# Kernel optimization log

Hardware: AMD Instinct MI355X
Metric: run time of the kernel (lower is better)

## Reference

```python
import jax, jax.numpy as jnp
import numpy as np

N = 8192
PERCENT_ON = 0.1
K = int(round(N * PERCENT_ON))  # 819
BOOST_STRENGTH = 1.0


def setup_inputs() -> dict:
    key = jax.random.key(0)
    k1, k2 = jax.random.split(key)
    x = jax.random.normal(k1, (4096, N), dtype=jnp.float32)
    duty_cycles = jax.random.uniform(k2, (N,), dtype=jnp.float32) * 0.2
    return {"x": x, "duty_cycles": duty_cycles}


def reference(x, duty_cycles):
    # boost factors: exp((target_density - duty_cycle) * boost_strength)
    boost_strength = jnp.maximum(jnp.float32(BOOST_STRENGTH), 0.0)
    target_density = jnp.float32(K / N)
    boost_factors = jnp.exp((target_density - duty_cycles) * boost_strength)
    boosted = x * boost_factors  # [B, N]
    # top-k on boosted values, but transmit ORIGINAL x values at winning units
    _, idx = jax.lax.top_k(boosted, K)  # idx: [B, K]
    updates = jnp.take_along_axis(x, idx, axis=1)  # [B, K]
    rows = jnp.arange(x.shape[0])[:, None]  # [B, 1]
    out = jnp.zeros_like(x).at[rows, idx].set(updates)
    return out
```

## Files before the change

kernel.cpp:

```cpp
#include <hip/hip_runtime.h>
#include <math.h>

#define NCOL 8192
#define NROW 4096
#define KSEL 819
#define TPB  256
#define VPT  8
#define LCAP 256
#define KPIV 0xBF866666u
#define NBKT 2048

typedef float f32x4 __attribute__((ext_vector_type(4)));

__device__ __align__(16) float g_boost[NCOL];

__global__ void boost_kernel(const float* __restrict__ duty) {
    int i = blockIdx.x * blockDim.x + threadIdx.x;
    if (i < NCOL) {
        float diff = (0.0999755859375f - duty[i]);
        g_boost[i] = (float)exp((double)diff);
    }
}

__device__ __forceinline__ unsigned f2k(float f) {
    unsigned u = __float_as_uint(f);
    return u ^ (0x80000000u | (unsigned)((int)u >> 31));
}

__device__ __forceinline__ int kbucket(unsigned k) {
    int b = (int)(k >> 13) - (int)(KPIV >> 13);
    return (b > NBKT - 1) ? (NBKT - 1) : b;
}

__global__ __launch_bounds__(TPB) void kwinners_kernel(const float* __restrict__ x,
                                                       float* __restrict__ out) {
    __shared__ __align__(16) unsigned char smem[16384];
    __shared__ int lds_wtot[4];
    __shared__ int lds_C, lds_cnt, lds_sel, lds_R1, lds_fE, lds_fR;
    __shared__ unsigned lds_th;

    int* hist = (int*)smem;
    unsigned* lkey = (unsigned*)(smem + 8192);

    const int t = threadIdx.x, row = blockIdx.x, lane = t & 63, w = t >> 6;
    const f32x4* x4 = (const f32x4*)(x + (size_t)row * NCOL);
    const f32x4* b4 = (const f32x4*)g_boost;

    unsigned kr[VPT][4];

    {
        int4* h4 = (int4*)hist;
        const int4 z = make_int4(0, 0, 0, 0);
        h4[2 * t] = z; h4[2 * t + 1] = z;
        if (t == 0) { lds_C = 0; lds_cnt = 0; lds_th = 0xFFFFFFFFu; }
    }

#pragma unroll
    for (int j = 0; j < VPT; ++j) {
        f32x4 xx = x4[t + TPB * j];
        f32x4 bb = b4[t + TPB * j];
        kr[j][0] = f2k(xx.x * bb.x);
        kr[j][1] = f2k(xx.y * bb.y);
        kr[j][2] = f2k(xx.z * bb.z);
        kr[j][3] = f2k(xx.w * bb.w);
    }
    __syncthreads();

    int cnt = 0;
#pragma unroll
    for (int j = 0; j < VPT; ++j)
#pragma unroll
        for (int c = 0; c < 4; ++c) {
            unsigned k = kr[j][c];
            if (k > KPIV) { ++cnt; atomicAdd(&hist[kbucket(k)], 1); }
        }
#pragma unroll
    for (int off = 32; off; off >>= 1) cnt += __shfl_down(cnt, off);
    if (lane == 0) atomicAdd(&lds_C, cnt);
    __syncthreads();
    const int C = lds_C;

    unsigned th = 0; int Rf = 0, E = 0; bool ok = false;

    if (C >= KSEL) {
        int arr[8];
        {
            int4 a0 = ((const int4*)hist)[2 * t];
            int4 a1 = ((const int4*)hist)[2 * t + 1];
            arr[0] = a0.x; arr[1] = a0.y; arr[2] = a0.z; arr[3] = a0.w;
            arr[4] = a1.x; arr[5] = a1.y; arr[6] = a1.z; arr[7] = a1.w;
        }
        int ts = arr[0] + arr[1] + arr[2] + arr[3] + arr[4] + arr[5] + arr[6] + arr[7];
        int s = ts;
#pragma unroll
        for (int off = 1; off < 64; off <<= 1) {
            int o = __shfl_down(s, off);
            if (lane + off < 64) s += o;
        }
        if (lane == 0) lds_wtot[w] = s;
        __syncthreads();
        int S_later = 0;
#pragma unroll
        for (int w2 = 0; w2 < 4; ++w2) if (w2 > w) S_later += lds_wtot[w2];
        const int S_ab = (s - ts) + S_later;
        if (S_ab < KSEL && S_ab + ts >= KSEL) {
            int cum = S_ab, selb = 0, r1 = 0;
#pragma unroll
            for (int b = 7; b >= 0; --b) {
                int nx = cum + arr[b];
                if (cum < KSEL && nx >= KSEL) { selb = 8 * t + b; r1 = KSEL - cum; }
                cum = nx;
            }
            lds_sel = selb; lds_R1 = r1;
        }
        __syncthreads();
        const int sel = lds_sel, R1 = lds_R1;

#pragma unroll
        for (int j = 0; j < VPT; ++j)
#pragma unroll
            for (int c = 0; c < 4; ++c) {
                unsigned k = kr[j][c];
                if (kbucket(k) == sel) {
                    int sl = atomicAdd(&lds_cnt, 1);
                    if (sl < LCAP) lkey[sl] = k;
                }
            }
        __syncthreads();
        const int n = lds_cnt;
        if (n <= LCAP) {
            if (t < n) {
                unsigned myk = lkey[t];
                int g = 0, e = 0;
                for (int i = 0; i < n; ++i) {
                    unsigned k2 = lkey[i];
                    g += (k2 > myk) ? 1 : 0;
                    e += (k2 == myk) ? 1 : 0;
                }
                if (g < R1 && g + e >= R1) lds_th = myk;
            }
            __syncthreads();
            th = lds_th;
            int ge = 0;
#pragma unroll
            for (int j = 0; j < VPT; ++j)
#pragma unroll
                for (int c = 0; c < 4; ++c) {
                    unsigned k = kr[j][c];
                    ge += (k > th ? 1 : 0) + (k == th ? (1 << 16) : 0);
                }
#pragma unroll
            for (int off = 32; off; off >>= 1) ge += __shfl_down(ge, off);
            if (lane == 0) lds_wtot[w] = ge;
            __syncthreads();
            const int GE = lds_wtot[0] + lds_wtot[1] + lds_wtot[2] + lds_wtot[3];
            const int G = GE & 0xFFFF, Eg = GE >> 16;
            if (G < KSEL && G + Eg >= KSEL) { ok = true; Rf = KSEL - G; E = Eg; }
        }
    }

    if (!ok) {
        unsigned prefix = 0; int R = KSEL;
        for (int p = 0; p < 4; ++p) {
            const int sh = 24 - 8 * p;
            hist[t] = 0;
            __syncthreads();
#pragma unroll
            for (int j = 0; j < VPT; ++j)
#pragma unroll
                for (int c = 0; c < 4; ++c) {
                    unsigned k = kr[j][c];
                    if (p == 0 || (k >> (sh + 8)) == (prefix >> (sh + 8)))
                        atomicAdd(&hist[(k >> sh) & 255u], 1);
                }
            __syncthreads();
            int h = hist[t], s2 = h;
#pragma unroll
            for (int off = 1; off < 64; off <<= 1) {
                int o = __shfl_down(s2, off);
                if (lane + off < 64) s2 += o;
            }
            if (lane == 0) lds_wtot[w] = s2;
            __syncthreads();
            int S_later = 0;
#pragma unroll
            for (int w2 = 0; w2 < 4; ++w2) if (w2 > w) S_later += lds_wtot[w2];
            const int S_ab = (s2 - h) + S_later;
            if (S_ab < R && S_ab + h >= R) { lds_sel = t; lds_fR = R - S_ab; lds_fE = h; }
            __syncthreads();
            prefix |= ((unsigned)lds_sel) << sh;
            R = lds_fR;
        }
        th = prefix; Rf = R; E = lds_fE;
    }

    unsigned dropm = 0;
    if (E > Rf) {
        unsigned short* tl = (unsigned short*)smem;
        __syncthreads();
        if (t == 0) lds_cnt = 0;
        __syncthreads();
#pragma unroll
        for (int j = 0; j < VPT; ++j)
#pragma unroll
            for (int c = 0; c < 4; ++c)
                if (kr[j][c] == th) {
                    int sl = atomicAdd(&lds_cnt, 1);
                    tl[sl] = (unsigned short)(4 * (t + TPB * j) + c);
                }
        __syncthreads();
        const int ntie = lds_cnt;
#pragma unroll
        for (int j = 0; j < VPT; ++j)
#pragma unroll
            for (int c = 0; c < 4; ++c)
                if (kr[j][c] == th) {
                    const int col = 4 * (t + TPB * j) + c;
                    int rank = 0;
                    for (int i = 0; i < ntie; ++i) rank += (tl[i] < col) ? 1 : 0;
                    if (rank >= Rf) dropm |= (1u << (4 * j + c));
                }
    }

    f32x4* o4 = (f32x4*)(out + (size_t)row * NCOL);
#pragma unroll
    for (int j = 0; j < VPT; ++j) {
        f32x4 xx = x4[t + TPB * j];
        f32x4 r;
        r.x = (kr[j][0] >= th && !((dropm >> (4 * j + 0)) & 1u)) ? xx.x : 0.0f;
        r.y = (kr[j][1] >= th && !((dropm >> (4 * j + 1)) & 1u)) ? xx.y : 0.0f;
        r.z = (kr[j][2] >= th && !((dropm >> (4 * j + 2)) & 1u)) ? xx.z : 0.0f;
        r.w = (kr[j][3] >= th && !((dropm >> (4 * j + 3)) & 1u)) ? xx.w : 0.0f;
        __builtin_nontemporal_store(r, &o4[t + TPB * j]);
    }
}

extern "C" void kernel_launch(void* const* d_in, const int* in_sizes, int n_in,
                              void* d_out, int out_size, void* d_ws, size_t ws_size,
                              hipStream_t stream) {
    const float* x = (const float*)d_in[0];
    const float* duty = (const float*)d_in[1];
    float* out = (float*)d_out;
    (void)in_sizes; (void)n_in; (void)out_size; (void)d_ws; (void)ws_size;

    boost_kernel<<<(NCOL + TPB - 1) / TPB, TPB, 0, stream>>>(duty);
    kwinners_kernel<<<NROW, TPB, 0, stream>>>(x, out);
}
```

Measured before the change: 63.76 us.

## Process two rows per block and stagger block start with a sleep

Each block now handles two rows in sequence, and the grid is halved. At start, each block spins on wall_clock64 with s_sleep for a hash-derived delay, so blocks enter their memory-heavy and compute phases at different times instead of all at once. The aim is to cut launch overhead and to spread load/compute phases across CUs for better overlap. The cost is fewer blocks for latency hiding, deliberate idle time at the start of most blocks, and an extra barrier between rows.

Measured after the change: 70.80 us. +11.0%, slower.

```diff
diff --git a/kernel.cpp b/kernel.cpp
--- a/kernel.cpp
+++ b/kernel.cpp
@@ -6,6 +6,7 @@
 #define KSEL 819
 #define TPB  256
 #define VPT  8
+#define RPB  2
 #define LCAP 256
 #define KPIV 0xBF866666u
 #define NBKT 2048
@@ -42,196 +43,211 @@
     int* hist = (int*)smem;
     unsigned* lkey = (unsigned*)(smem + 8192);
 
-    const int t = threadIdx.x, row = blockIdx.x, lane = t & 63, w = t >> 6;
-    const f32x4* x4 = (const f32x4*)(x + (size_t)row * NCOL);
+    const int t = threadIdx.x, lane = t & 63, w = t >> 6;
     const f32x4* b4 = (const f32x4*)g_boost;
 
-    unsigned kr[VPT][4];
-
     {
-        int4* h4 = (int4*)hist;
-        const int4 z = make_int4(0, 0, 0, 0);
-        h4[2 * t] = z; h4[2 * t + 1] = z;
-        if (t == 0) { lds_C = 0; lds_cnt = 0; lds_th = 0xFFFFFFFFu; }
+        const unsigned ph = ((unsigned)blockIdx.x * 2654435761u) >> 29;
+        if (ph) {
+            long long t0 = wall_clock64();
+            const long long tgt = (long long)ph * 40;
+            while (wall_clock64() - t0 < tgt) __builtin_amdgcn_s_sleep(8);
+        }
     }
 
-#pragma unroll
-    for (int j = 0; j < VPT; ++j) {
-        f32x4 xx = x4[t + TPB * j];
-        f32x4 bb = b4[t + TPB * j];
-        kr[j][0] = f2k(xx.x * bb.x);
-        kr[j][1] = f2k(xx.y * bb.y);
-        kr[j][2] = f2k(xx.z * bb.z);
-        kr[j][3] = f2k(xx.w * bb.w);
-    }
-    __syncthreads();
-
-    int cnt = 0;
-#pragma unroll
-    for (int j = 0; j < VPT; ++j)
-#pragma unroll
-        for (int c = 0; c < 4; ++c) {
-            unsigned k = kr[j][c];
-            if (k > KPIV) { ++cnt; atomicAdd(&hist[kbucket(k)], 1); }
-        }
-#pragma unroll
-    for (int off = 32; off; off >>= 1) cnt += __shfl_down(cnt, off);
-    if (lane == 0) atomicAdd(&lds_C, cnt);
-    __syncthreads();
-    const int C = lds_C;
-
-    unsigned th = 0; int Rf = 0, E = 0; bool ok = false;
-
-    if (C >= KSEL) {
-        int arr[8];
+    for (int r = 0; r < RPB; ++r) {
+        const int row = blockIdx.x * RPB + r;
+        const f32x4* x4 = (const f32x4*)(x + (size_t)row * NCOL);
+
+        unsigned kr[VPT][4];
+
         {
-            int4 a0 = ((const int4*)hist)[2 * t];
-            int4 a1 = ((const int4*)hist)[2 * t + 1];
-            arr[0] = a0.x; arr[1] = a0.y; arr[2] = a0.z; arr[3] = a0.w;
-            arr[4] = a1.x; arr[5] = a1.y; arr[6] = a1.z; arr[7] = a1.w;
-        }
-        int ts = arr[0] + arr[1] + arr[2] + arr[3] + arr[4] + arr[5] + arr[6] + arr[7];
-        int s = ts;
-#pragma unroll
-        for (int off = 1; off < 64; off <<= 1) {
-            int o = __shfl_down(s, off);
-            if (lane + off < 64) s += o;
-        }
-        if (lane == 0) lds_wtot[w] = s;
+            int4* h4 = (int4*)hist;
+            const int4 z = make_int4(0, 0, 0, 0);
+            h4[2 * t] = z; h4[2 * t + 1] = z;
+            if (t == 0) { lds_C = 0; lds_cnt = 0; lds_th = 0xFFFFFFFFu; }
+        }
+
+#pragma unroll
+        for (int j = 0; j < VPT; ++j) {
+            f32x4 xx = x4[t + TPB * j];
+            f32x4 bb = b4[t + TPB * j];
+            kr[j][0] = f2k(xx.x * bb.x);
+            kr[j][1] = f2k(xx.y * bb.y);
+            kr[j][2] = f2k(xx.z * bb.z);
+            kr[j][3] = f2k(xx.w * bb.w);
+        }
         __syncthreads();
-        int S_later = 0;
-#pragma unroll
-        for (int w2 = 0; w2 < 4; ++w2) if (w2 > w) S_later += lds_wtot[w2];
-        const int S_ab = (s - ts) + S_later;
-        if (S_ab < KSEL && S_ab + ts >= KSEL) {
-            int cum = S_ab, selb = 0, r1 = 0;
-#pragma unroll
-            for (int b = 7; b >= 0; --b) {
-                int nx = cum + arr[b];
-                if (cum < KSEL && nx >= KSEL) { selb = 8 * t + b; r1 = KSEL - cum; }
-                cum = nx;
-            }
-            lds_sel = selb; lds_R1 = r1;
-        }
-        __syncthreads();
-        const int sel = lds_sel, R1 = lds_R1;
-
+
+        int cnt = 0;
 #pragma unroll
         for (int j = 0; j < VPT; ++j)
 #pragma unroll
             for (int c = 0; c < 4; ++c) {
                 unsigned k = kr[j][c];
-                if (kbucket(k) == sel) {
-                    int sl = atomicAdd(&lds_cnt, 1);
-                    if (sl < LCAP) lkey[sl] = k;
-                }
-            }
+                if (k > KPIV) { ++cnt; atomicAdd(&hist[kbucket(k)], 1); }
+            }
+#pragma unroll
+        for (int off = 32; off; off >>= 1) cnt += __shfl_down(cnt, off);
+        if (lane == 0) atomicAdd(&lds_C, cnt);
         __syncthreads();
-        const int n = lds_cnt;
-        if (n <= LCAP) {
-            if (t < n) {
-                unsigned myk = lkey[t];
-                int g = 0, e = 0;
-                for (int i = 0; i < n; ++i) {
-                    unsigned k2 = lkey[i];
-                    g += (k2 > myk) ? 1 : 0;
-                    e += (k2 == myk) ? 1 : 0;
-                }
-                if (g < R1 && g + e >= R1) lds_th = myk;
-            }
-            __syncthreads();
-            th = lds_th;
-            int ge = 0;
+        const int C = lds_C;
+
+        unsigned th = 0; int Rf = 0, E = 0; bool ok = false;
+
+        if (C >= KSEL) {
+            int arr[8];
+            {
+                int4 a0 = ((const int4*)hist)[2 * t];
+                int4 a1 = ((const int4*)hist)[2 * t + 1];
+                arr[0] = a0.x; arr[1] = a0.y; arr[2] = a0.z; arr[3] = a0.w;
+                arr[4] = a1.x; arr[5] = a1.y; arr[6] = a1.z; arr[7] = a1.w;
+            }
+            int ts = arr[0] + arr[1] + arr[2] + arr[3] + arr[4] + arr[5] + arr[6] + arr[7];
+            int s = ts;
+#pragma unroll
+            for (int off = 1; off < 64; off <<= 1) {
+                int o = __shfl_down(s, off);
+                if (lane + off < 64) s += o;
+            }
+            if (lane == 0) lds_wtot[w] = s;
+            __syncthreads();
+            int S_later = 0;
+#pragma unroll
+            for (int w2 = 0; w2 < 4; ++w2) if (w2 > w) S_later += lds_wtot[w2];
+            const int S_ab = (s - ts) + S_later;
+            if (S_ab < KSEL && S_ab + ts >= KSEL) {
+                int cum = S_ab, selb = 0, r1 = 0;
+#pragma unroll
+                for (int b = 7; b >= 0; --b) {
+                    int nx = cum + arr[b];
+                    if (cum < KSEL && nx >= KSEL) { selb = 8 * t + b; r1 = KSEL - cum; }
+                    cum = nx;
+                }
+                lds_sel = selb; lds_R1 = r1;
+            }
+            __syncthreads();
+            const int sel = lds_sel, R1 = lds_R1;
+
 #pragma unroll
             for (int j = 0; j < VPT; ++j)
 #pragma unroll
                 for (int c = 0; c < 4; ++c) {
                     unsigned k = kr[j][c];
-                    ge += (k > th ? 1 : 0) + (k == th ? (1 << 16) : 0);
-                }
-#pragma unroll
-            for (int off = 32; off; off >>= 1) ge += __shfl_down(ge, off);
-            if (lane == 0) lds_wtot[w] = ge;
-            __syncthreads();
-            const int GE = lds_wtot[0] + lds_wtot[1] + lds_wtot[2] + lds_wtot[3];
-            const int G = GE & 0xFFFF, Eg = GE >> 16;
-            if (G < KSEL && G + Eg >= KSEL) { ok = true; Rf = KSEL - G; E = Eg; }
-        }
-    }
-
-    if (!ok) {
-        unsigned prefix = 0; int R = KSEL;
-        for (int p = 0; p < 4; ++p) {
-            const int sh = 24 - 8 * p;
-            hist[t] = 0;
+                    if (kbucket(k) == sel) {
+                        int sl = atomicAdd(&lds_cnt, 1);
+                        if (sl < LCAP) lkey[sl] = k;
+                    }
+                }
+            __syncthreads();
+            const int n = lds_cnt;
+            if (n <= LCAP) {
+                if (t < n) {
+                    unsigned myk = lkey[t];
+                    int g = 0, e = 0;
+                    for (int i = 0; i < n; ++i) {
+                        unsigned k2 = lkey[i];
+                        g += (k2 > myk) ? 1 : 0;
+                        e += (k2 == myk) ? 1 : 0;
+                    }
+                    if (g < R1 && g + e >= R1) lds_th = myk;
+                }
+                __syncthreads();
+                th = lds_th;
+                int ge = 0;
+#pragma unroll
+                for (int j = 0; j < VPT; ++j)
+#pragma unroll
+                    for (int c = 0; c < 4; ++c) {
+                        unsigned k = kr[j][c];
+                        ge += (k > th ? 1 : 0) + (k == th ? (1 << 16) : 0);
+                    }
+#pragma unroll
+                for (int off = 32; off; off >>= 1) ge += __shfl_down(ge, off);
+                if (lane == 0) lds_wtot[w] = ge;
+                __syncthreads();
+                const int GE = lds_wtot[0] + lds_wtot[1] + lds_wtot[2] + lds_wtot[3];
+                const int G = GE & 0xFFFF, Eg = GE >> 16;
+                if (G < KSEL && G + Eg >= KSEL) { ok = true; Rf = KSEL - G; E = Eg; }
+            }
+        }
+
+        if (!ok) {
+            unsigned prefix = 0; int R = KSEL;
+            for (int p = 0; p < 4; ++p) {
+                const int sh = 24 - 8 * p;
+                hist[t] = 0;
+                __syncthreads();
+#pragma unroll
+                for (int j = 0; j < VPT; ++j)
+#pragma unroll
+                    for (int c = 0; c < 4; ++c) {
+                        unsigned k = kr[j][c];
+                        if (p == 0 || (k >> (sh + 8)) == (prefix >> (sh + 8)))
+                            atomicAdd(&hist[(k >> sh) & 255u], 1);
+                    }
+                __syncthreads();
+                int h = hist[t], s2 = h;
+#pragma unroll
+                for (int off = 1; off < 64; off <<= 1) {
+                    int o = __shfl_down(s2, off);
+                    if (lane + off < 64) s2 += o;
+                }
+                if (lane == 0) lds_wtot[w] = s2;
+                __syncthreads();
+                int S_later = 0;
+#pragma unroll
+                for (int w2 = 0; w2 < 4; ++w2) if (w2 > w) S_later += lds_wtot[w2];
+                const int S_ab = (s2 - h) + S_later;
+                if (S_ab < R && S_ab + h >= R) { lds_sel = t; lds_fR = R - S_ab; lds_fE = h; }
+                __syncthreads();
+                prefix |= ((unsigned)lds_sel) << sh;
+                R = lds_fR;
+            }
+            th = prefix; Rf = R; E = lds_fE;
+        }
+
+        unsigned dropm = 0;
+        if (E > Rf) {
+            unsigned short* tl = (unsigned short*)smem;
+            __syncthreads();
+            if (t == 0) lds_cnt = 0;
             __syncthreads();
 #pragma unroll
             for (int j = 0; j < VPT; ++j)
 #pragma unroll
-                for (int c = 0; c < 4; ++c) {
-                    unsigned k = kr[j][c];
-                    if (p == 0 || (k >> (sh + 8)) == (prefix >> (sh + 8)))
-                        atomicAdd(&hist[(k >> sh) & 255u], 1);
-                }
-            __syncthreads();
-            int h = hist[t], s2 = h;
-#pragma unroll
-            for (int off = 1; off < 64; off <<= 1) {
-                int o = __shfl_down(s2, off);
-                if (lane + off < 64) s2 += o;
-            }
-            if (lane == 0) lds_wtot[w] = s2;
-            __syncthreads();
-            int S_later = 0;
-#pragma unroll
-            for (int w2 = 0; w2 < 4; ++w2) if (w2 > w) S_later += lds_wtot[w2];
-            const int S_ab = (s2 - h) + S_later;
-            if (S_ab < R && S_ab + h >= R) { lds_sel = t; lds_fR = R - S_ab; lds_fE = h; }
-            __syncthreads();
-            prefix |= ((unsigned)lds_sel) << sh;
-            R = lds_fR;
-        }
-        th = prefix; Rf = R; E = lds_fE;
-    }
-
-    unsigned dropm = 0;
-    if (E > Rf) {
-        unsigned short* tl = (unsigned short*)smem;
+                for (int c = 0; c < 4; ++c)
+                    if (kr[j][c] == th) {
+                        int sl = atomicAdd(&lds_cnt, 1);
+                        tl[sl] = (unsigned short)(4 * (t + TPB * j) + c);
+                    }
+            __syncthreads();
+            const int ntie = lds_cnt;
+#pragma unroll
+            for (int j = 0; j < VPT; ++j)
+#pragma unroll
+                for (int c = 0; c < 4; ++c)
+                    if (kr[j][c] == th) {
+                        const int col = 4 * (t + TPB * j) + c;
+                        int rank = 0;
+                        for (int i = 0; i < ntie; ++i) rank += (tl[i] < col) ? 1 : 0;
+                        if (rank >= Rf) dropm |= (1u << (4 * j + c));
+                    }
+        }
+
+        f32x4* o4 = (f32x4*)(out + (size_t)row * NCOL);
+#pragma unroll
+        for (int j = 0; j < VPT; ++j) {
+            f32x4 xx = x4[t + TPB * j];
+            f32x4 rr;
+            rr.x = (kr[j][0] >= th && !((dropm >> (4 * j + 0)) & 1u)) ? xx.x : 0.0f;
+            rr.y = (kr[j][1] >= th && !((dropm >> (4 * j + 1)) & 1u)) ? xx.y : 0.0f;
+            rr.z = (kr[j][2] >= th && !((dropm >> (4 * j + 2)) & 1u)) ? xx.z : 0.0f;
+            rr.w = (kr[j][3] >= th && !((dropm >> (4 * j + 3)) & 1u)) ? xx.w : 0.0f;
+            __builtin_nontemporal_store(rr, &o4[t + TPB * j]);
+        }
+
         __syncthreads();
-        if (t == 0) lds_cnt = 0;
-        __syncthreads();
-#pragma unroll
-        for (int j = 0; j < VPT; ++j)
-#pragma unroll
-            for (int c = 0; c < 4; ++c)
-                if (kr[j][c] == th) {
-                    int sl = atomicAdd(&lds_cnt, 1);
-                    tl[sl] = (unsigned short)(4 * (t + TPB * j) + c);
-                }
-        __syncthreads();
-        const int ntie = lds_cnt;
-#pragma unroll
-        for (int j = 0; j < VPT; ++j)
-#pragma unroll
-            for (int c = 0; c < 4; ++c)
-                if (kr[j][c] == th) {
-                    const int col = 4 * (t + TPB * j) + c;
-                    int rank = 0;
-                    for (int i = 0; i < ntie; ++i) rank += (tl[i] < col) ? 1 : 0;
-                    if (rank >= Rf) dropm |= (1u << (4 * j + c));
-                }
-    }
-
-    f32x4* o4 = (f32x4*)(out + (size_t)row * NCOL);
-#pragma unroll
-    for (int j = 0; j < VPT; ++j) {
-        f32x4 xx = x4[t + TPB * j];
-        f32x4 r;
-        r.x = (kr[j][0] >= th && !((dropm >> (4 * j + 0)) & 1u)) ? xx.x : 0.0f;
-        r.y = (kr[j][1] >= th && !((dropm >> (4 * j + 1)) & 1u)) ? xx.y : 0.0f;
-        r.z = (kr[j][2] >= th && !((dropm >> (4 * j + 2)) & 1u)) ? xx.z : 0.0f;
-        r.w = (kr[j][3] >= th && !((dropm >> (4 * j + 3)) & 1u)) ? xx.w : 0.0f;
-        __builtin_nontemporal_store(r, &o4[t + TPB * j]);
     }
 }
 
@@ -243,6 +259,6 @@
     float* out = (float*)d_out;
     (void)in_sizes; (void)n_in; (void)out_size; (void)d_ws; (void)ws_size;
 
-    boost_kernel<<<(NCOL + TPB - 1) / TPB, TPB, 0, stream>>>(duty);
-    kwinners_kernel<<<NROW, TPB, 0, stream>>>(x, out);
-}
+    boost_kernel<<<(NCOL + 255) / 256, 256, 0, stream>>>(duty);
+    kwinners_kernel<<<NROW / RPB, TPB, 0, stream>>>(x, out);
+}
```
